# Performance work log

Hardware: AMD Instinct MI355X
Metric: run time of the kernel (lower is better)

Reference implementation:

```python
import jax, jax.numpy as jnp
import numpy as np
from jax import lax

# Model constants (from init_kwargs + canonical Mamba defaults)
VOCAB = 32000
D_MODEL = 512
N_LAYERS = 6
D_INNER = 2 * D_MODEL          # expand=2
D_STATE = 16
D_CONV = 4
DT_RANK = D_MODEL // 16        # 32
B, L = 2, 1024
EPS = 1e-5


def setup_inputs() -> dict:
    key = jax.random.key(0)
    ks = jax.random.split(key, 12)
    s = 0.02
    # A initialized as in mamba_ssm: A = 1..d_state repeated over channels
    A = jnp.tile(jnp.arange(1, D_STATE + 1, dtype=jnp.float32), (D_INNER, 1))  # [d_inner, d_state]
    A_log = jnp.tile(jnp.log(A)[None], (N_LAYERS, 1, 1))
    return {
        "tokens": jax.random.randint(ks[0], (B, L), 0, VOCAB),
        "embed": jax.random.normal(ks[1], (VOCAB, D_MODEL), jnp.float32) * s,
        "in_proj_w": jax.random.normal(ks[2], (N_LAYERS, 2 * D_INNER, D_MODEL), jnp.float32) * s,
        "conv_w": jax.random.normal(ks[3], (N_LAYERS, D_INNER, 1, D_CONV), jnp.float32) * 0.2,
        "conv_b": jnp.zeros((N_LAYERS, D_INNER), jnp.float32),
        "x_proj_w": jax.random.normal(ks[4], (N_LAYERS, DT_RANK + 2 * D_STATE, D_INNER), jnp.float32) * s,
        "dt_proj_w": jax.random.normal(ks[5], (N_LAYERS, D_INNER, DT_RANK), jnp.float32) * 0.1,
        "dt_proj_b": jnp.full((N_LAYERS, D_INNER), -4.0, jnp.float32),  # softplus -> small dt
        "A_log": A_log,
        "D_skip": jnp.ones((N_LAYERS, D_INNER), jnp.float32),
        "out_proj_w": jax.random.normal(ks[6], (N_LAYERS, D_MODEL, D_INNER), jnp.float32) * s,
        "norm_w": jnp.ones((D_MODEL,), jnp.float32),
        "norm_b": jnp.zeros((D_MODEL,), jnp.float32),
        "head_w": jax.random.normal(ks[7], (VOCAB, D_MODEL), jnp.float32) * s,
    }


def _selective_scan(dA, dBu, C):
    # dA, dBu: [b, l, d, n]; C: [b, l, n] -> y: [b, l, d]
    def step(h, inp):
        dA_t, dBu_t, c_t = inp          # [b,d,n], [b,d,n], [b,n]
        h = dA_t * h + dBu_t
        return h, jnp.einsum("bdn,bn->bd", h, c_t)
    h0 = jnp.zeros(dA.shape[:1] + dA.shape[2:], dA.dtype)  # [b, d, n]
    _, ys = lax.scan(step, h0, (jnp.moveaxis(dA, 1, 0), jnp.moveaxis(dBu, 1, 0), jnp.moveaxis(C, 1, 0)))
    return jnp.moveaxis(ys, 0, 1)


def _mamba_block(x, inw, cw, cb, xpw, dtw, dtb, A_log, Dp, outw):
    # x: [b, l, d_model]
    xz = jnp.einsum("bld,ed->ble", x, inw)            # [b, l, 2*d_inner]
    xi, z = jnp.split(xz, 2, axis=-1)                  # each [b, l, d_inner]
    # causal depthwise conv1d
    xc = jnp.moveaxis(xi, 1, 2)                        # [b, d_inner, l]
    xc = lax.conv_general_dilated(xc, cw, (1,), [(D_CONV - 1, 0)],
                                  feature_group_count=D_INNER)
    xi = jax.nn.silu(jnp.moveaxis(xc + cb[None, :, None], 1, 2))  # [b, l, d_inner]
    # input-dependent dt, B, C
    dbc = jnp.einsum("bld,ed->ble", xi, xpw)           # [b, l, dt_rank+2*d_state]
    dt, Bm, Cm = jnp.split(dbc, [DT_RANK, DT_RANK + D_STATE], axis=-1)
    delta = jax.nn.softplus(jnp.einsum("blr,dr->bld", dt, dtw) + dtb)  # [b, l, d_inner]
    A = -jnp.exp(A_log)                                # [d_inner, d_state]
    dA = jnp.exp(delta[..., None] * A)                 # [b, l, d_inner, d_state]
    dBu = (delta * xi)[..., None] * Bm[:, :, None, :]  # [b, l, d_inner, d_state]
    y = _selective_scan(dA, dBu, Cm) + xi * Dp         # [b, l, d_inner]
    y = y * jax.nn.silu(z)
    return jnp.einsum("ble,de->bld", y, outw)          # [b, l, d_model]


def reference(tokens, embed, in_proj_w, conv_w, conv_b, x_proj_w, dt_proj_w,
              dt_proj_b, A_log, D_skip, out_proj_w, norm_w, norm_b, head_w):
    x = embed[tokens]                                  # [b, l, d_model]
    for i in range(N_LAYERS):
        x = _mamba_block(x, in_proj_w[i], conv_w[i], conv_b[i], x_proj_w[i],
                         dt_proj_w[i], dt_proj_b[i], A_log[i], D_skip[i], out_proj_w[i])
    mu = jnp.mean(x, axis=-1, keepdims=True)
    var = jnp.mean(jnp.square(x - mu), axis=-1, keepdims=True)
    x = (x - mu) * lax.rsqrt(var + EPS) * norm_w + norm_b
    logits = jnp.einsum("bld,vd->blv", x, head_w)      # [b, l, vocab]
    return logits
```

## Files before the change

kernel.cpp:

```cpp
#include <hip/hip_runtime.h>
#include <hip/hip_bf16.h>
#include <cstdint>
#include <cstddef>

#define VOCAB 32000
#define DMODEL 512
#define NLAYERS 6
#define DINNER 1024
#define DSTATE 16
#define DCONV 4
#define DTRANK 32
#define BB 2
#define LL 1024
#define ROWS (BB * LL)
#define CHUNK 64
#define NCH 16

typedef _Float16 half8 __attribute__((ext_vector_type(8)));
typedef float floatx4 __attribute__((ext_vector_type(4)));

__device__ __forceinline__ void gload16(const _Float16* g, _Float16* l) {
    __builtin_amdgcn_global_load_lds(
        (const __attribute__((address_space(1))) unsigned int*)g,
        (__attribute__((address_space(3))) unsigned int*)l, 16, 0, 0);
}

__global__ __launch_bounds__(128) void embed_k(const int* __restrict__ tokens,
                                               const float* __restrict__ embed,
                                               float* __restrict__ x) {
    int row = blockIdx.x;
    int tid = threadIdx.x;
    int tok = tokens[row];
    *(float4*)(x + (size_t)row * DMODEL + tid * 4) =
        *(const float4*)(embed + (size_t)tok * DMODEL + tid * 4);
}

template<int BM, int BN, int MODE>
__global__ __launch_bounds__(256) void gemm_split(
    const float* __restrict__ A, int lda,
    const float* __restrict__ W, int ldw,
    float* __restrict__ C, int ldc,
    int K, int NBX)
{
    constexpr int FM = BM / 32;
    constexpr int FN = BN / 32;
    constexpr int ACH = BM * 4;
    constexpr int TOT = (BM + BN) * 4;
    constexpr int CH = TOT / 256;
    __shared__ __attribute__((aligned(16))) _Float16 As[2][BM * 64];
    __shared__ __attribute__((aligned(16))) _Float16 Bs[2][BN * 64];

    int bid = blockIdx.x;
    int bx, by;
    if (MODE == 1) {
        int xcd = bid & 7, j = bid >> 3;
        bx = xcd * 32 + (j >> 4);
        by = j & 15;
        if (bx >= NBX) return;
    } else {
        int cpx = gridDim.x >> 3;
        int swz = (bid & 7) * cpx + (bid >> 3);
        bx = swz % NBX;
        by = swz / NBX;
    }
    int m0 = by * BM, n0 = bx * BN;

    int tid = threadIdx.x;
    int wid = tid >> 6, lane = tid & 63;
    int wm = wid >> 1, wn = wid & 1;
    int lr = lane & 15, lk = lane >> 4;

    floatx4 acc[FM][FN] = {};
    float4 p0[CH], p1[CH];

    auto LOAD = [&](int k0) {
#pragma unroll
        for (int c = 0; c < CH; ++c) {
            int i = tid + c * 256;
            bool isA = i < ACH;
            int jj = isA ? i : i - ACH;
            int r = jj >> 2, c8 = jj & 3;
            const float* src = isA ? (A + (size_t)(m0 + r) * lda + k0 + c8 * 8)
                                   : (W + (size_t)(n0 + r) * ldw + k0 + c8 * 8);
            p0[c] = *(const float4*)(src);
            p1[c] = *(const float4*)(src + 4);
        }
    };
    auto STORE = [&](int buf) {
#pragma unroll
        for (int c = 0; c < CH; ++c) {
            int i = tid + c * 256;
            bool isA = i < ACH;
            int jj = isA ? i : i - ACH;
            int r = jj >> 2, c8 = jj & 3;
            float vv[8] = {p0[c].x, p0[c].y, p0[c].z, p0[c].w,
                           p1[c].x, p1[c].y, p1[c].z, p1[c].w};
            half8 hi, lo;
#pragma unroll
            for (int e = 0; e < 8; ++e) {
                _Float16 h = (_Float16)vv[e];
                hi[e] = h;
                lo[e] = (_Float16)(vv[e] - (float)h);
            }
            _Float16* dst = (isA ? As[buf] : Bs[buf]) + r * 64;
            *(half8*)(dst + (((c8)     ^ (r & 7)) << 3)) = hi;
            *(half8*)(dst + (((c8 + 4) ^ (r & 7)) << 3)) = lo;
        }
    };

    LOAD(0);
    STORE(0);
    int cur = 0;
    for (int k0 = 0; k0 < K; k0 += 32) {
        __syncthreads();
        if (k0 + 32 < K) LOAD(k0 + 32);

        half8 ah[FM], al[FM], bh[FN], bl[FN];
#pragma unroll
        for (int f = 0; f < FM; ++f) {
            int r = wm * (BM / 2) + f * 16 + lr;
            const _Float16* p = As[cur] + r * 64;
            ah[f] = *(const half8*)(p + (((lk)     ^ (r & 7)) << 3));
            al[f] = *(const half8*)(p + (((lk + 4) ^ (r & 7)) << 3));
        }
#pragma unroll
        for (int f = 0; f < FN; ++f) {
            int r = wn * (BN / 2) + f * 16 + lr;
            const _Float16* p = Bs[cur] + r * 64;
            bh[f] = *(const half8*)(p + (((lk)     ^ (r & 7)) << 3));
            bl[f] = *(const half8*)(p + (((lk + 4) ^ (r & 7)) << 3));
        }
#pragma unroll
        for (int i2 = 0; i2 < FM; ++i2)
#pragma unroll
            for (int j2 = 0; j2 < FN; ++j2) {
                acc[i2][j2] = __builtin_amdgcn_mfma_f32_16x16x32_f16(ah[i2], bh[j2], acc[i2][j2], 0, 0, 0);
                acc[i2][j2] = __builtin_amdgcn_mfma_f32_16x16x32_f16(ah[i2], bl[j2], acc[i2][j2], 0, 0, 0);
                acc[i2][j2] = __builtin_amdgcn_mfma_f32_16x16x32_f16(al[i2], bh[j2], acc[i2][j2], 0, 0, 0);
            }
        if (k0 + 32 < K) STORE(cur ^ 1);
        cur ^= 1;
    }

#pragma unroll
    for (int f = 0; f < FM; ++f)
#pragma unroll
        for (int g = 0; g < FN; ++g) {
            int row = m0 + wm * (BM / 2) + f * 16 + (lane >> 4) * 4;
            int col = n0 + wn * (BN / 2) + g * 16 + (lane & 15);
#pragma unroll
            for (int j = 0; j < 4; ++j)
                C[(size_t)(row + j) * ldc + col] = acc[f][g][j];
        }
}

__global__ __launch_bounds__(256) void gemm_nt(
    const float* __restrict__ A, int lda,
    const float* __restrict__ W, int ldw,
    float* __restrict__ C, int ldc,
    int M, int N, int K)
{
    __shared__ float As[16][64];
    __shared__ float Bs[16][64];
    int tid = threadIdx.x;
    int tx = tid & 15, ty = tid >> 4;
    int m0 = blockIdx.y * 64, n0 = blockIdx.x * 64;
    int lr = tid >> 2;
    int lc = (tid & 3) * 4;
    float acc[4][4] = {};

    for (int k0 = 0; k0 < K; k0 += 16) {
        float4 a4 = *(const float4*)(A + (size_t)(m0 + lr) * lda + k0 + lc);
        float4 b4 = *(const float4*)(W + (size_t)(n0 + lr) * ldw + k0 + lc);
        As[lc + 0][lr] = a4.x; As[lc + 1][lr] = a4.y;
        As[lc + 2][lr] = a4.z; As[lc + 3][lr] = a4.w;
        Bs[lc + 0][lr] = b4.x; Bs[lc + 1][lr] = b4.y;
        Bs[lc + 2][lr] = b4.z; Bs[lc + 3][lr] = b4.w;
        __syncthreads();
#pragma unroll
        for (int k = 0; k < 16; ++k) {
            float4 av = *(const float4*)&As[k][ty * 4];
            float4 bv = *(const float4*)&Bs[k][tx * 4];
            float a_[4] = {av.x, av.y, av.z, av.w};
            float b_[4] = {bv.x, bv.y, bv.z, bv.w};
#pragma unroll
            for (int i = 0; i < 4; ++i)
#pragma unroll
                for (int j = 0; j < 4; ++j)
                    acc[i][j] += a_[i] * b_[j];
        }
        __syncthreads();
    }

#pragma unroll
    for (int i = 0; i < 4; ++i) {
        float4 o = {acc[i][0], acc[i][1], acc[i][2], acc[i][3]};
        *(float4*)(C + (size_t)(m0 + ty * 4 + i) * ldc + n0 + tx * 4) = o;
    }
}

__global__ __launch_bounds__(256) void conv_silu(const float* __restrict__ xz,
                                                 const float* __restrict__ cw,
                                                 const float* __restrict__ cb,
                                                 float* __restrict__ xi) {
    int idx = blockIdx.x * 256 + threadIdx.x;
    int d = idx & 1023;
    int t = (idx >> 10) & 1023;
    int b = idx >> 20;
    const float* base = xz + (size_t)(b * LL) * (2 * DINNER) + d;
    float acc = cb[d];
#pragma unroll
    for (int j = 0; j < DCONV; ++j) {
        int tt = t - 3 + j;
        if (tt >= 0) acc += cw[d * 4 + j] * base[(size_t)tt * (2 * DINNER)];
    }
    xi[idx] = acc / (1.f + expf(-acc));
}

template <int PASS>
__global__ __launch_bounds__(256) void scan_k(
    const float* __restrict__ xi, const float* __restrict__ dbc,
    const float* __restrict__ dtw, const float* __restrict__ dtb,
    const float* __restrict__ A_log, const float* __restrict__ Dskip,
    const float* __restrict__ xz,
    float* __restrict__ P, float* __restrict__ S,
    const float* __restrict__ H0, float* __restrict__ yg)
{
    __shared__ float sd[CHUNK][16], sx[CHUNK][16], sB[CHUNK][16];
    __shared__ float ovraw[CHUNK * 32];
    __shared__ float sdtT[32][16];
    __shared__ float sdtb[16];
    float (*db)[32] = (float(*)[32])ovraw;
    float (*sC)[16] = (float(*)[16])ovraw;
    float (*sY)[16] = (float(*)[16])(ovraw + CHUNK * 16);

    int c = blockIdx.x, dblk = blockIdx.y, b = blockIdx.z;
    int tid = threadIdx.x;
    int d0 = dblk * 16, t0 = c * CHUNK;

    for (int idx = tid; idx < 512; idx += 256)
        sdtT[idx >> 4][idx & 15] = dtw[(size_t)(d0 + (idx & 15)) * DTRANK + (idx >> 4)];
    if (tid < 16) sdtb[tid] = dtb[d0 + tid];
    for (int idx = tid; idx < CHUNK * 16; idx += 256) {
        int t = idx >> 4, i = idx & 15;
        size_t row = (size_t)(b * LL + t0 + t);
        sx[t][i] = xi[row * DINNER + d0 + i];
        sB[t][i] = dbc[row * 64 + DTRANK + i];
    }
    for (int idx = tid; idx < CHUNK * 8; idx += 256) {
        int t = idx >> 3, q = idx & 7;
        size_t row = (size_t)(b * LL + t0 + t);
        *(float4*)&db[t][q * 4] = *(const float4*)(dbc + row * 64 + q * 4);
    }
    __syncthreads();

    for (int idx = tid; idx < CHUNK * 16; idx += 256) {
        int t = idx >> 4, i = idx & 15;
        float a = sdtb[i];
#pragma unroll
        for (int k = 0; k < DTRANK; ++k) a += db[t][k] * sdtT[k][i];
        sd[t][i] = (a > 20.f) ? a : log1pf(expf(a));
    }
    __syncthreads();

    if (PASS == 3) {
        for (int idx = tid; idx < CHUNK * 16; idx += 256) {
            int t = idx >> 4, i = idx & 15;
            size_t row = (size_t)(b * LL + t0 + t);
            sC[t][i] = dbc[row * 64 + DTRANK + DSTATE + i];
        }
        __syncthreads();
    }

    int di = tid >> 4, n = tid & 15;
    int d = d0 + di;
    float Adn = -expf(A_log[d * DSTATE + n]);
    float Dsk = Dskip[d];
    float h = (PASS == 1) ? 0.f : H0[(size_t)(c * 2 + b) * 16384 + d * 16 + n];
    float ap = 1.f;

    for (int t = 0; t < CHUNK; ++t) {
        float dl = sd[t][di];
        float dA = expf(dl * Adn);
        h = dA * h + dl * sx[t][di] * sB[t][n];
        if (PASS == 1) {
            ap *= dA;
        } else {
            float p = h * sC[t][n];
            p += __shfl_xor(p, 1);
            p += __shfl_xor(p, 2);
            p += __shfl_xor(p, 4);
            p += __shfl_xor(p, 8);
            if (n == 0) sY[t][di] = p + sx[t][di] * Dsk;
        }
    }

    if (PASS == 1) {
        size_t o = (size_t)(c * 2 + b) * 16384 + d * 16 + n;
        P[o] = ap;
        S[o] = h;
    } else {
        __syncthreads();
        for (int idx = tid; idx < CHUNK * 16; idx += 256) {
            int t = idx >> 4, i = idx & 15;
            size_t row = (size_t)(b * LL + t0 + t);
            float z = xz[row * (2 * DINNER) + DINNER + d0 + i];
            yg[row * DINNER + d0 + i] = sY[t][i] * (z / (1.f + expf(-z)));
        }
    }
}

__global__ __launch_bounds__(256) void scan_carry(const float* __restrict__ P,
                                                  const float* __restrict__ S,
                                                  float* __restrict__ H0) {
    int idx = blockIdx.x * 256 + threadIdx.x;
    float carry = 0.f;
#pragma unroll
    for (int c = 0; c < NCH; ++c) {
        H0[(size_t)c * 32768 + idx] = carry;
        carry = P[(size_t)c * 32768 + idx] * carry + S[(size_t)c * 32768 + idx];
    }
}

__global__ __launch_bounds__(128) void lnorm(const float* __restrict__ x,
                                             const float* __restrict__ w,
                                             const float* __restrict__ bp,
                                             float* __restrict__ xn) {
    int row = blockIdx.x;
    int tid = threadIdx.x;
    float4 v = *(const float4*)(x + (size_t)row * DMODEL + tid * 4);
    float s = v.x + v.y + v.z + v.w;
    float q = v.x * v.x + v.y * v.y + v.z * v.z + v.w * v.w;
#pragma unroll
    for (int m = 1; m < 64; m <<= 1) {
        s += __shfl_xor(s, m);
        q += __shfl_xor(q, m);
    }
    __shared__ float ss[2], qq[2];
    if ((tid & 63) == 0) { ss[tid >> 6] = s; qq[tid >> 6] = q; }
    __syncthreads();
    s = ss[0] + ss[1];
    q = qq[0] + qq[1];
    float mu = s / (float)DMODEL;
    float var = q / (float)DMODEL - mu * mu;
    float r = rsqrtf(var + 1e-5f);
    int c = tid * 4;
    float4 o;
    o.x = (v.x - mu) * r * w[c + 0] + bp[c + 0];
    o.y = (v.y - mu) * r * w[c + 1] + bp[c + 1];
    o.z = (v.z - mu) * r * w[c + 2] + bp[c + 2];
    o.w = (v.w - mu) * r * w[c + 3] + bp[c + 3];
    *(float4*)(xn + (size_t)row * DMODEL + c) = o;
}

__global__ __launch_bounds__(256) void split16(const float* __restrict__ src,
                                               _Float16* __restrict__ hi,
                                               _Float16* __restrict__ lo,
                                               int NT) {
    int g = blockIdx.x * 256 + threadIdx.x;
    int lane = g & 63;
    int tl = g >> 6;
    int nt = tl % NT, kc = tl / NT;
    int n = nt * 16 + (lane & 15);
    int k = kc * 32 + (lane >> 4) * 8;
    const float* s = src + (size_t)n * 512 + k;
    float4 v0 = *(const float4*)(s);
    float4 v1 = *(const float4*)(s + 4);
    float vv[8] = {v0.x, v0.y, v0.z, v0.w, v1.x, v1.y, v1.z, v1.w};
    half8 h, l;
#pragma unroll
    for (int e = 0; e < 8; ++e) {
        _Float16 hh = (_Float16)vv[e];
        h[e] = hh;
        l[e] = (_Float16)(vv[e] - (float)hh);
    }
    *(half8*)(hi + (size_t)g * 8) = h;
    *(half8*)(lo + (size_t)g * 8) = l;
}

__global__ __launch_bounds__(256) void gemm_head(
    const _Float16* __restrict__ Ah, const _Float16* __restrict__ Al,
    const _Float16* __restrict__ Wh, const _Float16* __restrict__ Wl,
    float* __restrict__ C)
{
    __shared__ __attribute__((aligned(16))) _Float16 lds[2][4][8][512];
    int bid = blockIdx.x;
    int xcd = bid & 7, j = bid >> 3;
    int bx = xcd * 32 + (j >> 4);
    int by = j & 15;
    if (bx >= 250) return;

    int tid = threadIdx.x;
    int wid = tid >> 6, lane = tid & 63;
    int wm = wid >> 1, wn = wid & 1;
    floatx4 acc[4][4] = {};

    auto STAGE = [&](int buf, int kc) {
        int t0 = wid * 2;
#pragma unroll
        for (int t = t0; t < t0 + 2; ++t) {
            size_t ao = ((size_t)kc * 128 + by * 8 + t) * 512 + lane * 8;
            size_t bo = ((size_t)kc * 2000 + bx * 8 + t) * 512 + lane * 8;
            gload16(Ah + ao, &lds[buf][0][t][0]);
            gload16(Al + ao, &lds[buf][1][t][0]);
            gload16(Wh + bo, &lds[buf][2][t][0]);
            gload16(Wl + bo, &lds[buf][3][t][0]);
        }
    };

    STAGE(0, 0);
    __syncthreads();
    int cur = 0;
    for (int kc = 0; kc < 16; ++kc) {
        if (kc < 15) STAGE(cur ^ 1, kc + 1);
        half8 ah[4], al[4], bh[4], bl[4];
#pragma unroll
        for (int f = 0; f < 4; ++f) {
            ah[f] = *(const half8*)&lds[cur][0][wm * 4 + f][lane * 8];
            al[f] = *(const half8*)&lds[cur][1][wm * 4 + f][lane * 8];
            bh[f] = *(const half8*)&lds[cur][2][wn * 4 + f][lane * 8];
            bl[f] = *(const half8*)&lds[cur][3][wn * 4 + f][lane * 8];
        }
#pragma unroll
        for (int f = 0; f < 4; ++f)
#pragma unroll
            for (int g = 0; g < 4; ++g) {
                acc[f][g] = __builtin_amdgcn_mfma_f32_16x16x32_f16(ah[f], bh[g], acc[f][g], 0, 0, 0);
                acc[f][g] = __builtin_amdgcn_mfma_f32_16x16x32_f16(ah[f], bl[g], acc[f][g], 0, 0, 0);
                acc[f][g] = __builtin_amdgcn_mfma_f32_16x16x32_f16(al[f], bh[g], acc[f][g], 0, 0, 0);
            }
        __syncthreads();
        cur ^= 1;
    }

#pragma unroll
    for (int f = 0; f < 4; ++f)
#pragma unroll
        for (int g = 0; g < 4; ++g) {
            int row = by * 128 + wm * 64 + f * 16 + (lane >> 4) * 4;
            int col = bx * 128 + wn * 64 + g * 16 + (lane & 15);
#pragma unroll
            for (int jj = 0; jj < 4; ++jj)
                C[(size_t)(row + jj) * VOCAB + col] = acc[f][g][jj];
        }
}

extern "C" void kernel_launch(void* const* d_in, const int* in_sizes, int n_in,
                              void* d_out, int out_size, void* d_ws, size_t ws_size,
                              hipStream_t stream) {
    const int*   tokens = (const int*)d_in[0];
    const float* embed  = (const float*)d_in[1];
    const float* inw    = (const float*)d_in[2];
    const float* cw     = (const float*)d_in[3];
    const float* cb     = (const float*)d_in[4];
    const float* xpw    = (const float*)d_in[5];
    const float* dtw    = (const float*)d_in[6];
    const float* dtb    = (const float*)d_in[7];
    const float* Alog   = (const float*)d_in[8];
    const float* Dsk    = (const float*)d_in[9];
    const float* outw   = (const float*)d_in[10];
    const float* nw     = (const float*)d_in[11];
    const float* nb     = (const float*)d_in[12];
    const float* hw     = (const float*)d_in[13];
    float* out = (float*)d_out;

    float* ws = (float*)d_ws;
    float* xn  = ws;
    float* x   = ws + (1u << 20);
    float* xz  = ws + (2u << 20);
    float* xib = ws + (6u << 20);
    float* dbc = ws + (8u << 20);
    float* yg  = dbc + (1 << 17);
    float* Pb  = yg + (2u << 20);
    float* Sb  = Pb + (1 << 19);
    float* H0  = Sb + (1 << 19);

    _Float16* Hbase = (_Float16*)(ws + (1u << 20));
    _Float16* Wh = Hbase;
    _Float16* Wl = Wh + (size_t)VOCAB * 512;
    _Float16* Ahh = Wl + (size_t)VOCAB * 512;
    _Float16* All = Ahh + (size_t)ROWS * 512;
    bool fast_head = ws_size >= (size_t)74 * 1024 * 1024;

    embed_k<<<ROWS, 128, 0, stream>>>(tokens, embed, x);

    for (int l = 0; l < NLAYERS; ++l) {
        const float* inw_l  = inw  + (size_t)l * 2 * DINNER * DMODEL;
        const float* cw_l   = cw   + (size_t)l * DINNER * DCONV;
        const float* cb_l   = cb   + (size_t)l * DINNER;
        const float* xpw_l  = xpw  + (size_t)l * 64 * DINNER;
        const float* dtw_l  = dtw  + (size_t)l * DINNER * DTRANK;
        const float* dtb_l  = dtb  + (size_t)l * DINNER;
        const float* Alog_l = Alog + (size_t)l * DINNER * DSTATE;
        const float* Dsk_l  = Dsk  + (size_t)l * DINNER;
        const float* outw_l = outw + (size_t)l * DMODEL * DINNER;

        gemm_split<128, 128, 0><<<16 * 16, 256, 0, stream>>>(
            x, DMODEL, inw_l, DMODEL, xz, 2 * DINNER, DMODEL, 16);
        conv_silu<<<(ROWS * DINNER) / 256, 256, 0, stream>>>(xz, cw_l, cb_l, xib);
        gemm_nt<<<dim3(1, ROWS / 64), 256, 0, stream>>>(
            xib, DINNER, xpw_l, DINNER, dbc, 64, ROWS, 64, DINNER);
        scan_k<1><<<dim3(NCH, DINNER / 16, BB), 256, 0, stream>>>(
            xib, dbc, dtw_l, dtb_l, Alog_l, Dsk_l, xz, Pb, Sb, nullptr, nullptr);
        scan_carry<<<128, 256, 0, stream>>>(Pb, Sb, H0);
        scan_k<3><<<dim3(NCH, DINNER / 16, BB), 256, 0, stream>>>(
            xib, dbc, dtw_l, dtb_l, Alog_l, Dsk_l, xz, nullptr, nullptr, H0, yg);
        gemm_split<64, 64, 0><<<32 * 8, 256, 0, stream>>>(
            yg, DINNER, outw_l, DINNER, x, DMODEL, DINNER, 8);
    }

    lnorm<<<ROWS, 128, 0, stream>>>(x, nw, nb, xn);

    if (fast_head) {
        split16<<<8000, 256, 0, stream>>>(hw, Wh, Wl, VOCAB / 16);
        split16<<<512, 256, 0, stream>>>(xn, Ahh, All, ROWS / 16);
        gemm_head<<<4096, 256, 0, stream>>>(Ahh, All, Wh, Wl, out);
    } else {
        gemm_split<128, 128, 1><<<4096, 256, 0, stream>>>(
            xn, DMODEL, hw, DMODEL, out, VOCAB, DMODEL, 250);
    }
}
```

Baseline: 1.758 ms.

## Replace chunked two-pass scan with single-pass scan and split-K MFMA x_proj

Removes the three-kernel chunked scan (partial pass, carry kernel, second pass) and replaces it with one kernel that walks the whole sequence serially per channel block, so the recomputation and extra launches go away. The scalar x_proj GEMM becomes a split-K MFMA gemm_split mode that writes four partial outputs, which the scan sums while loading. The in_proj GEMM tile is also shrunk to 64x128 to launch more blocks. The single-pass scan has only 128 blocks, each with a long serial loop, so parallelism drops sharply and latency could rise.

```diff
diff --git a/kernel.cpp b/kernel.cpp
--- a/kernel.cpp
+++ b/kernel.cpp
@@ -13,8 +13,6 @@
 #define BB 2
 #define LL 1024
 #define ROWS (BB * LL)
-#define CHUNK 64
-#define NCH 16
 
 typedef _Float16 half8 __attribute__((ext_vector_type(8)));
 typedef float floatx4 __attribute__((ext_vector_type(4)));
@@ -52,11 +50,21 @@
 
     int bid = blockIdx.x;
     int bx, by;
+    int koff = 0;
+    size_t cof = 0;
     if (MODE == 1) {
         int xcd = bid & 7, j = bid >> 3;
         bx = xcd * 32 + (j >> 4);
         by = j & 15;
         if (bx >= NBX) return;
+    } else if (MODE == 2) {
+        int cpx = gridDim.x >> 3;
+        int swz = (bid & 7) * cpx + (bid >> 3);
+        by = swz & 15;
+        int kc = swz >> 4;
+        bx = 0;
+        koff = kc * 256;
+        cof = (size_t)kc * ROWS * 64;
     } else {
         int cpx = gridDim.x >> 3;
         int swz = (bid & 7) * cpx + (bid >> 3);
@@ -80,8 +88,8 @@
             bool isA = i < ACH;
             int jj = isA ? i : i - ACH;
             int r = jj >> 2, c8 = jj & 3;
-            const float* src = isA ? (A + (size_t)(m0 + r) * lda + k0 + c8 * 8)
-                                   : (W + (size_t)(n0 + r) * ldw + k0 + c8 * 8);
+            const float* src = isA ? (A + (size_t)(m0 + r) * lda + koff + k0 + c8 * 8)
+                                   : (W + (size_t)(n0 + r) * ldw + koff + k0 + c8 * 8);
             p0[c] = *(const float4*)(src);
             p1[c] = *(const float4*)(src + 4);
         }
@@ -150,53 +158,8 @@
             int col = n0 + wn * (BN / 2) + g * 16 + (lane & 15);
 #pragma unroll
             for (int j = 0; j < 4; ++j)
-                C[(size_t)(row + j) * ldc + col] = acc[f][g][j];
-        }
-}
-
-__global__ __launch_bounds__(256) void gemm_nt(
-    const float* __restrict__ A, int lda,
-    const float* __restrict__ W, int ldw,
-    float* __restrict__ C, int ldc,
-    int M, int N, int K)
-{
-    __shared__ float As[16][64];
-    __shared__ float Bs[16][64];
-    int tid = threadIdx.x;
-    int tx = tid & 15, ty = tid >> 4;
-    int m0 = blockIdx.y * 64, n0 = blockIdx.x * 64;
-    int lr = tid >> 2;
-    int lc = (tid & 3) * 4;
-    float acc[4][4] = {};
-
-    for (int k0 = 0; k0 < K; k0 += 16) {
-        float4 a4 = *(const float4*)(A + (size_t)(m0 + lr) * lda + k0 + lc);
-        float4 b4 = *(const float4*)(W + (size_t)(n0 + lr) * ldw + k0 + lc);
-        As[lc + 0][lr] = a4.x; As[lc + 1][lr] = a4.y;
-        As[lc + 2][lr] = a4.z; As[lc + 3][lr] = a4.w;
-        Bs[lc + 0][lr] = b4.x; Bs[lc + 1][lr] = b4.y;
-        Bs[lc + 2][lr] = b4.z; Bs[lc + 3][lr] = b4.w;
-        __syncthreads();
-#pragma unroll
-        for (int k = 0; k < 16; ++k) {
-            float4 av = *(const float4*)&As[k][ty * 4];
-            float4 bv = *(const float4*)&Bs[k][tx * 4];
-            float a_[4] = {av.x, av.y, av.z, av.w};
-            float b_[4] = {bv.x, bv.y, bv.z, bv.w};
-#pragma unroll
-            for (int i = 0; i < 4; ++i)
-#pragma unroll
-                for (int j = 0; j < 4; ++j)
-                    acc[i][j] += a_[i] * b_[j];
-        }
-        __syncthreads();
-    }
-
-#pragma unroll
-    for (int i = 0; i < 4; ++i) {
-        float4 o = {acc[i][0], acc[i][1], acc[i][2], acc[i][3]};
-        *(float4*)(C + (size_t)(m0 + ty * 4 + i) * ldc + n0 + tx * 4) = o;
-    }
+                C[cof + (size_t)(row + j) * ldc + col] = acc[f][g][j];
+        }
 }
 
 __global__ __launch_bounds__(256) void conv_silu(const float* __restrict__ xz,
@@ -217,75 +180,62 @@
     xi[idx] = acc / (1.f + expf(-acc));
 }
 
-template <int PASS>
-__global__ __launch_bounds__(256) void scan_k(
-    const float* __restrict__ xi, const float* __restrict__ dbc,
+__global__ __launch_bounds__(256) void scan_full(
+    const float* __restrict__ xi, const float* __restrict__ dbcp,
     const float* __restrict__ dtw, const float* __restrict__ dtb,
     const float* __restrict__ A_log, const float* __restrict__ Dskip,
-    const float* __restrict__ xz,
-    float* __restrict__ P, float* __restrict__ S,
-    const float* __restrict__ H0, float* __restrict__ yg)
+    const float* __restrict__ xz, float* __restrict__ yg)
 {
-    __shared__ float sd[CHUNK][16], sx[CHUNK][16], sB[CHUNK][16];
-    __shared__ float ovraw[CHUNK * 32];
+    #define TCH 128
+    __shared__ float sd[TCH][16], sx[TCH][16], sB[TCH][16], sC[TCH][16];
+    __shared__ float ovraw[TCH * 32];
     __shared__ float sdtT[32][16];
     __shared__ float sdtb[16];
     float (*db)[32] = (float(*)[32])ovraw;
-    float (*sC)[16] = (float(*)[16])ovraw;
-    float (*sY)[16] = (float(*)[16])(ovraw + CHUNK * 16);
-
-    int c = blockIdx.x, dblk = blockIdx.y, b = blockIdx.z;
+    float (*sY)[16] = (float(*)[16])ovraw;
+
+    int dblk = blockIdx.x, b = blockIdx.y;
     int tid = threadIdx.x;
-    int d0 = dblk * 16, t0 = c * CHUNK;
+    int d0 = dblk * 16;
 
     for (int idx = tid; idx < 512; idx += 256)
         sdtT[idx >> 4][idx & 15] = dtw[(size_t)(d0 + (idx & 15)) * DTRANK + (idx >> 4)];
     if (tid < 16) sdtb[tid] = dtb[d0 + tid];
-    for (int idx = tid; idx < CHUNK * 16; idx += 256) {
-        int t = idx >> 4, i = idx & 15;
-        size_t row = (size_t)(b * LL + t0 + t);
-        sx[t][i] = xi[row * DINNER + d0 + i];
-        sB[t][i] = dbc[row * 64 + DTRANK + i];
-    }
-    for (int idx = tid; idx < CHUNK * 8; idx += 256) {
-        int t = idx >> 3, q = idx & 7;
-        size_t row = (size_t)(b * LL + t0 + t);
-        *(float4*)&db[t][q * 4] = *(const float4*)(dbc + row * 64 + q * 4);
-    }
-    __syncthreads();
-
-    for (int idx = tid; idx < CHUNK * 16; idx += 256) {
-        int t = idx >> 4, i = idx & 15;
-        float a = sdtb[i];
-#pragma unroll
-        for (int k = 0; k < DTRANK; ++k) a += db[t][k] * sdtT[k][i];
-        sd[t][i] = (a > 20.f) ? a : log1pf(expf(a));
-    }
-    __syncthreads();
-
-    if (PASS == 3) {
-        for (int idx = tid; idx < CHUNK * 16; idx += 256) {
-            int t = idx >> 4, i = idx & 15;
-            size_t row = (size_t)(b * LL + t0 + t);
-            sC[t][i] = dbc[row * 64 + DTRANK + DSTATE + i];
-        }
-        __syncthreads();
-    }
 
     int di = tid >> 4, n = tid & 15;
     int d = d0 + di;
     float Adn = -expf(A_log[d * DSTATE + n]);
     float Dsk = Dskip[d];
-    float h = (PASS == 1) ? 0.f : H0[(size_t)(c * 2 + b) * 16384 + d * 16 + n];
-    float ap = 1.f;
-
-    for (int t = 0; t < CHUNK; ++t) {
-        float dl = sd[t][di];
-        float dA = expf(dl * Adn);
-        h = dA * h + dl * sx[t][di] * sB[t][n];
-        if (PASS == 1) {
-            ap *= dA;
-        } else {
+    float h = 0.f;
+
+    for (int c = 0; c < LL / TCH; ++c) {
+        int t0 = c * TCH;
+        for (int idx = tid; idx < TCH * 16; idx += 256) {
+            int t = idx >> 4, i = idx & 15;
+            sx[t][i] = xi[(size_t)(b * LL + t0 + t) * DINNER + d0 + i];
+        }
+        for (int idx = tid; idx < TCH * 64; idx += 256) {
+            int t = idx >> 6, j = idx & 63;
+            size_t o = (size_t)(b * LL + t0 + t) * 64 + j;
+            float v = dbcp[o] + dbcp[(size_t)ROWS * 64 + o]
+                    + dbcp[(size_t)2 * ROWS * 64 + o] + dbcp[(size_t)3 * ROWS * 64 + o];
+            if (j < DTRANK)            db[t][j] = v;
+            else if (j < DTRANK + 16)  sB[t][j - DTRANK] = v;
+            else                       sC[t][j - DTRANK - 16] = v;
+        }
+        __syncthreads();
+        for (int idx = tid; idx < TCH * 16; idx += 256) {
+            int t = idx >> 4, i = idx & 15;
+            float a = sdtb[i];
+#pragma unroll
+            for (int k = 0; k < DTRANK; ++k) a += db[t][k] * sdtT[k][i];
+            sd[t][i] = (a > 20.f) ? a : log1pf(expf(a));
+        }
+        __syncthreads();
+        for (int t = 0; t < TCH; ++t) {
+            float dl = sd[t][di];
+            float dA = expf(dl * Adn);
+            h = dA * h + dl * sx[t][di] * sB[t][n];
             float p = h * sC[t][n];
             p += __shfl_xor(p, 1);
             p += __shfl_xor(p, 2);
@@ -293,33 +243,16 @@
             p += __shfl_xor(p, 8);
             if (n == 0) sY[t][di] = p + sx[t][di] * Dsk;
         }
-    }
-
-    if (PASS == 1) {
-        size_t o = (size_t)(c * 2 + b) * 16384 + d * 16 + n;
-        P[o] = ap;
-        S[o] = h;
-    } else {
-        __syncthreads();
-        for (int idx = tid; idx < CHUNK * 16; idx += 256) {
+        __syncthreads();
+        for (int idx = tid; idx < TCH * 16; idx += 256) {
             int t = idx >> 4, i = idx & 15;
             size_t row = (size_t)(b * LL + t0 + t);
             float z = xz[row * (2 * DINNER) + DINNER + d0 + i];
             yg[row * DINNER + d0 + i] = sY[t][i] * (z / (1.f + expf(-z)));
         }
-    }
-}
-
-__global__ __launch_bounds__(256) void scan_carry(const float* __restrict__ P,
-                                                  const float* __restrict__ S,
-                                                  float* __restrict__ H0) {
-    int idx = blockIdx.x * 256 + threadIdx.x;
-    float carry = 0.f;
-#pragma unroll
-    for (int c = 0; c < NCH; ++c) {
-        H0[(size_t)c * 32768 + idx] = carry;
-        carry = P[(size_t)c * 32768 + idx] * carry + S[(size_t)c * 32768 + idx];
-    }
+        __syncthreads();
+    }
+    #undef TCH
 }
 
 __global__ __launch_bounds__(128) void lnorm(const float* __restrict__ x,
@@ -465,18 +398,14 @@
     float* out = (float*)d_out;
 
     float* ws = (float*)d_ws;
-    float* xn  = ws;
-    float* x   = ws + (1u << 20);
-    float* xz  = ws + (2u << 20);
-    float* xib = ws + (6u << 20);
-    float* dbc = ws + (8u << 20);
-    float* yg  = dbc + (1 << 17);
-    float* Pb  = yg + (2u << 20);
-    float* Sb  = Pb + (1 << 19);
-    float* H0  = Sb + (1 << 19);
-
-    _Float16* Hbase = (_Float16*)(ws + (1u << 20));
-    _Float16* Wh = Hbase;
+    float* xn   = ws;
+    float* x    = ws + (1u << 20);
+    float* xz   = ws + (2u << 20);
+    float* xib  = ws + (6u << 20);
+    float* dbcp = ws + (8u << 20);
+    float* yg   = dbcp + (1u << 19);
+
+    _Float16* Wh = (_Float16*)(ws + (1u << 20));
     _Float16* Wl = Wh + (size_t)VOCAB * 512;
     _Float16* Ahh = Wl + (size_t)VOCAB * 512;
     _Float16* All = Ahh + (size_t)ROWS * 512;
@@ -495,16 +424,13 @@
         const float* Dsk_l  = Dsk  + (size_t)l * DINNER;
         const float* outw_l = outw + (size_t)l * DMODEL * DINNER;
 
-        gemm_split<128, 128, 0><<<16 * 16, 256, 0, stream>>>(
+        gemm_split<64, 128, 0><<<32 * 16, 256, 0, stream>>>(
             x, DMODEL, inw_l, DMODEL, xz, 2 * DINNER, DMODEL, 16);
         conv_silu<<<(ROWS * DINNER) / 256, 256, 0, stream>>>(xz, cw_l, cb_l, xib);
-        gemm_nt<<<dim3(1, ROWS / 64), 256, 0, stream>>>(
-            xib, DINNER, xpw_l, DINNER, dbc, 64, ROWS, 64, DINNER);
-        scan_k<1><<<dim3(NCH, DINNER / 16, BB), 256, 0, stream>>>(
-            xib, dbc, dtw_l, dtb_l, Alog_l, Dsk_l, xz, Pb, Sb, nullptr, nullptr);
-        scan_carry<<<128, 256, 0, stream>>>(Pb, Sb, H0);
-        scan_k<3><<<dim3(NCH, DINNER / 16, BB), 256, 0, stream>>>(
-            xib, dbc, dtw_l, dtb_l, Alog_l, Dsk_l, xz, nullptr, nullptr, H0, yg);
+        gemm_split<128, 64, 2><<<64, 256, 0, stream>>>(
+            xib, DINNER, xpw_l, DINNER, dbcp, 64, 256, 16);
+        scan_full<<<dim3(DINNER / 16, BB), 256, 0, stream>>>(
+            xib, dbcp, dtw_l, dtb_l, Alog_l, Dsk_l, xz, yg);
         gemm_split<64, 64, 0><<<32 * 8, 256, 0, stream>>>(
             yg, DINNER, outw_l, DINNER, x, DMODEL, DINNER, 8);
     }
```

New measurement: 3.321 ms. 88.9% more time.
